# Optimization experiments

Measured on AMD Instinct MI355X. Metric: run time of the kernel, lower is better.

## Reference

```python
import jax, jax.numpy as jnp
import numpy as np

DIM = 512
NUM_HEADS = 8
HEAD_DIM = DIM // NUM_HEADS


def setup_inputs() -> dict:
    key = jax.random.key(0)
    ks = jax.random.split(key, 5)
    s = 0.02
    x = jax.random.normal(ks[0], (2, 4096, DIM), dtype=jnp.float32)
    W_qkv = jax.random.normal(ks[1], (DIM, 3 * DIM), dtype=jnp.float32) * s
    b_qkv = jnp.zeros((3 * DIM,), dtype=jnp.float32)
    W_proj = jax.random.normal(ks[2], (DIM, DIM), dtype=jnp.float32) * s
    b_proj = jnp.zeros((DIM,), dtype=jnp.float32)
    return {"x": x, "W_qkv": W_qkv, "b_qkv": b_qkv, "W_proj": W_proj, "b_proj": b_proj}


def reference(x, W_qkv, b_qkv, W_proj, b_proj):
    B, N, C = x.shape
    # qkv: [B,N,3C] -> [3,B,H,N,Dh]
    qkv = (x @ W_qkv + b_qkv).reshape(B, N, 3, NUM_HEADS, HEAD_DIM)
    qkv = jnp.transpose(qkv, (2, 0, 3, 1, 4))
    q, k, v = qkv[0], qkv[1], qkv[2]
    scale = HEAD_DIM ** -0.5
    # naive full attention matrix [B,H,N,N] (faithful to source)
    attn = jnp.einsum('bhqd,bhkd->bhqk', q, k) * scale
    attn = jax.nn.softmax(attn, axis=-1)
    out = jnp.einsum('bhqk,bhkd->bhqd', attn, v)  # [B,H,N,Dh]
    out = jnp.transpose(out, (0, 2, 1, 3)).reshape(B, N, C)
    return out @ W_proj + b_proj
```

## Files before the change

### kernel.cpp

```cpp
#include <hip/hip_runtime.h>
#include <stdint.h>

typedef _Float16 f16;
typedef _Float16 f16x4 __attribute__((ext_vector_type(4)));
typedef _Float16 f16x8 __attribute__((ext_vector_type(8)));
typedef float f32x4 __attribute__((ext_vector_type(4)));
typedef float f32x16 __attribute__((ext_vector_type(16)));
typedef uint32_t u32;
typedef u32 u32x2 __attribute__((ext_vector_type(2)));
typedef u32 u32x4 __attribute__((ext_vector_type(4)));

#define NHEADS 8
#define DH 64
#define BATCH 2
#define SEQ 4096
#define CDIM 512
#define MTOT (BATCH * SEQ)
#define QSCALE 0.18033688011112042f

__device__ __forceinline__ void gload_lds16(const void* g, void* l) {
  __builtin_amdgcn_global_load_lds(
      (const __attribute__((address_space(1))) uint32_t*)g,
      (__attribute__((address_space(3))) uint32_t*)l, 16, 0, 0);
}

__device__ __forceinline__ u32 pk2(float a, float b) {
  auto h = __builtin_amdgcn_cvt_pkrtz(a, b);
  return __builtin_bit_cast(u32, h);
}

__device__ __forceinline__ void pl32swap(u32& a, u32& b) {
  asm volatile("v_permlane32_swap_b32 %0, %1" : "+v"(a), "+v"(b));
}

__global__ void cvt_f32_f16(const float* __restrict__ in, f16* __restrict__ outp, int n) {
  int i = (blockIdx.x * 256 + threadIdx.x) * 4;
  if (i < n) {
    float4 v = *(const float4*)(in + i);
    f16x4 o = {(f16)v.x, (f16)v.y, (f16)v.z, (f16)v.w};
    *(f16x4*)(outp + i) = o;
  }
}

__global__ void cvt_transpose(const float* __restrict__ src, f16* __restrict__ dst, int Kd, int Nd) {
  int i = blockIdx.x * 256 + threadIdx.x;
  if (i < Kd * Nd) {
    int k = i / Nd, n = i - k * Nd;
    dst[(size_t)n * Kd + k] = (f16)src[i];
  }
}

template <int MODE>
__global__ __launch_bounds__(256) void gemm_f16(
    const f16* __restrict__ A, const f16* __restrict__ Bt,
    const float* __restrict__ bias, int Ncols,
    f16* __restrict__ Qo, f16* __restrict__ Ko, f16* __restrict__ Vo,
    float* __restrict__ Fo) {
  const int K = CDIM;
  const int nTN = Ncols >> 7;
  const int bm = blockIdx.x / nTN, bn = blockIdx.x % nTN;
  const int M0 = bm << 7, N0 = bn << 7;
  __shared__ __align__(16) char ldsA[128 * 64 * 2];
  __shared__ __align__(16) char ldsB[128 * 64 * 2];
  const int t = threadIdx.x;
  const int w = t >> 6, lane = t & 63;
  const int wr = w >> 1, wc = w & 1;
  const int lm = lane & 15, lk = lane >> 4;
  f32x4 acc[4][4] = {};

  const int srow = t >> 3;
  const int sj = t & 7;

  for (int k0 = 0; k0 < K; k0 += 64) {
    __syncthreads();
#pragma unroll
    for (int q = 0; q < 4; ++q) {
      int row = (q << 5) + srow;
      int col = (sj ^ (row & 7)) << 3;
      gload_lds16(A + (size_t)(M0 + row) * K + k0 + col,
                  ldsA + ((q << 8) + (w << 6)) * 16);
      gload_lds16(Bt + (size_t)(N0 + row) * K + k0 + col,
                  ldsB + ((q << 8) + (w << 6)) * 16);
    }
    asm volatile("s_waitcnt vmcnt(0)" ::: "memory");
    __syncthreads();
#pragma unroll
    for (int h = 0; h < 2; ++h) {
      f16x8 af[4], bf[4];
#pragma unroll
      for (int mi = 0; mi < 4; ++mi) {
        int row = (wr << 6) + (mi << 4) + lm;
        int slot = ((h << 2) + lk) ^ (row & 7);
        af[mi] = *(const f16x8*)(ldsA + row * 128 + slot * 16);
      }
#pragma unroll
      for (int ni = 0; ni < 4; ++ni) {
        int row = (wc << 6) + (ni << 4) + lm;
        int slot = ((h << 2) + lk) ^ (row & 7);
        bf[ni] = *(const f16x8*)(ldsB + row * 128 + slot * 16);
      }
#pragma unroll
      for (int mi = 0; mi < 4; ++mi)
#pragma unroll
        for (int ni = 0; ni < 4; ++ni)
          acc[mi][ni] = __builtin_amdgcn_mfma_f32_16x16x32_f16(af[mi], bf[ni], acc[mi][ni], 0, 0, 0);
    }
  }

  const int cbase = N0 + (wc << 6);
  if (MODE == 0) {
    const int tsec = cbase >> 9;
    const int hh = (cbase & 511) >> 6;
#pragma unroll
    for (int mi = 0; mi < 4; ++mi)
#pragma unroll
      for (int ni = 0; ni < 4; ++ni) {
        int c = cbase + (ni << 4) + lm;
        int d = c & 63;
        float bv = bias[c];
#pragma unroll
        for (int r = 0; r < 4; ++r) {
          int m = M0 + (wr << 6) + (mi << 4) + (lk << 2) + r;
          float v = acc[mi][ni][r] + bv;
          int bb = m >> 12, tok = m & 4095;
          size_t bh = (size_t)bb * NHEADS + hh;
          if (tsec == 0)      Qo[(bh * SEQ + tok) * DH + d] = (f16)(v * QSCALE);
          else if (tsec == 1) Ko[(bh * SEQ + tok) * DH + d] = (f16)v;
          else                Vo[(bh * DH + d) * SEQ + tok] = (f16)v;
        }
      }
  } else {
#pragma unroll
    for (int mi = 0; mi < 4; ++mi)
#pragma unroll
      for (int ni = 0; ni < 4; ++ni) {
        int c = cbase + (ni << 4) + lm;
        float bv = bias[c];
#pragma unroll
        for (int r = 0; r < 4; ++r) {
          int m = M0 + (wr << 6) + (mi << 4) + (lk << 2) + r;
          Fo[(size_t)m * CDIM + c] = acc[mi][ni][r] + bv;
        }
      }
  }
}

__global__ __launch_bounds__(256, 2) void attn_f16(
    const f16* __restrict__ Qw, const f16* __restrict__ Kw,
    const f16* __restrict__ Vw, f16* __restrict__ Ao) {
  const int bh = blockIdx.x >> 5;
  const int qt = blockIdx.x & 31;
  const int t = threadIdx.x, lane = t & 63;
  const int l31 = lane & 31, hi = lane >> 5;
  const int w = t >> 6;
  const int p = w & 1;
  const int wq = w >> 1;
  __shared__ __align__(16) char lds[65536];
  const int qbase = (qt << 7) + (wq << 6);
  const int qA = qbase + l31;
  const int qB = qbase + 32 + l31;
  const f16* QbA = Qw + ((size_t)bh * SEQ + qA) * DH;
  const f16* QbB = Qw + ((size_t)bh * SEQ + qB) * DH;
  f16x8 qfA[4], qfB[4];
#pragma unroll
  for (int cd = 0; cd < 4; ++cd) {
    qfA[cd] = *(const f16x8*)(QbA + cd * 16 + hi * 8);
    qfB[cd] = *(const f16x8*)(QbB + cd * 16 + hi * 8);
  }
  f32x16 oA0 = {}, oA1 = {}, oB0 = {}, oB1 = {};
  float lA = 0.f, lB = 0.f;
  const f16* Kb = Kw + (size_t)bh * SEQ * DH;
  const f16* Vb = Vw + (size_t)bh * DH * SEQ;
  const int srow = t >> 3, sj = t & 7;

#define STAGE(buf, kv0_)                                                      \
  {                                                                           \
    _Pragma("unroll") for (int q2 = 0; q2 < 2; ++q2) {                        \
      const int row = (q2 << 5) + srow;                                       \
      const int col = (sj ^ (row & 7)) << 3;                                  \
      gload_lds16(Kb + (size_t)((kv0_) + row) * DH + col,                     \
                  lds + (buf) * 16384 + row * 128 + sj * 16);                 \
      gload_lds16(Vb + (size_t)row * SEQ + (kv0_) + col,                      \
                  lds + 32768 + (buf) * 16384 + row * 128 + sj * 16);         \
    }                                                                         \
  }

  STAGE(0, 0);
  __syncthreads();

#pragma unroll 2
  for (int tt = 0; tt < 64; ++tt) {
    const int cur = tt & 1;
    const char* Kc = lds + cur * 16384;
    const char* Vc = lds + 32768 + cur * 16384;
    if (tt < 63) STAGE(cur ^ 1, (tt + 1) << 6);

    f16x8 kf[4];
    const int krow = (p << 5) + l31;
#pragma unroll
    for (int cd = 0; cd < 4; ++cd)
      kf[cd] = *(const f16x8*)(Kc + krow * 128 + ((((cd << 1) | hi) ^ (l31 & 7)) << 4));

    f32x16 sA = {}, sB = {};
#pragma unroll
    for (int cd = 0; cd < 4; ++cd) {
      sA = __builtin_amdgcn_mfma_f32_32x32x16_f16(kf[cd], qfA[cd], sA, 0, 0, 0);
      sB = __builtin_amdgcn_mfma_f32_32x32x16_f16(kf[cd], qfB[cd], sB, 0, 0, 0);
    }

    f16x8 pfA[2], pfB[2];
#define SOFTMAX(s, l, pf)                                                     \
    {                                                                         \
      _Pragma("unroll") for (int i = 0; i < 16; ++i)                          \
          s[i] = __builtin_amdgcn_exp2f(s[i]);                                \
      float a8[8];                                                            \
      _Pragma("unroll") for (int i = 0; i < 8; ++i) a8[i] = s[i] + s[i + 8];  \
      l += ((a8[0] + a8[1]) + (a8[2] + a8[3])) +                              \
           ((a8[4] + a8[5]) + (a8[6] + a8[7]));                               \
      _Pragma("unroll") for (int c = 0; c < 2; ++c) {                         \
        u32 a0 = pk2(s[8 * c + 0], s[8 * c + 1]);                             \
        u32 a1 = pk2(s[8 * c + 2], s[8 * c + 3]);                             \
        u32 b0 = pk2(s[8 * c + 4], s[8 * c + 5]);                             \
        u32 b1 = pk2(s[8 * c + 6], s[8 * c + 7]);                             \
        pl32swap(a0, b0);                                                     \
        pl32swap(a1, b1);                                                     \
        u32x4 pw = {a0, a1, b0, b1};                                          \
        pf[c] = __builtin_bit_cast(f16x8, pw);                                \
      }                                                                       \
    }
    SOFTMAX(sA, lA, pfA);
    SOFTMAX(sB, lB, pfB);

    f16x8 vf0[2], vf1[2];
#pragma unroll
    for (int c2 = 0; c2 < 2; ++c2) {
      const int ck = (p << 1) | c2;
      const int sl = (((ck << 1) | hi) ^ (l31 & 7)) << 4;
      vf0[c2] = *(const f16x8*)(Vc + l31 * 128 + sl);
      vf1[c2] = *(const f16x8*)(Vc + (32 + l31) * 128 + sl);
    }
#pragma unroll
    for (int c2 = 0; c2 < 2; ++c2) {
      oA0 = __builtin_amdgcn_mfma_f32_32x32x16_f16(vf0[c2], pfA[c2], oA0, 0, 0, 0);
      oA1 = __builtin_amdgcn_mfma_f32_32x32x16_f16(vf1[c2], pfA[c2], oA1, 0, 0, 0);
      oB0 = __builtin_amdgcn_mfma_f32_32x32x16_f16(vf0[c2], pfB[c2], oB0, 0, 0, 0);
      oB1 = __builtin_amdgcn_mfma_f32_32x32x16_f16(vf1[c2], pfB[c2], oB1, 0, 0, 0);
    }
    __syncthreads();
  }

  float* ob = (float*)(lds) + (((wq << 6) + lane) << 5);
  float* mlb = (float*)(lds + 16384) + ((wq << 6) + lane);
  const int b_ = bh >> 3, h_ = bh & 7;

#define MERGE_WRITE(o0, o1, l, myq)                                           \
    {                                                                         \
      if (p) {                                                                \
        *(f32x16*)ob = o0;                                                    \
        *(f32x16*)(ob + 16) = o1;                                             \
        mlb[0] = l;                                                           \
      }                                                                       \
      __syncthreads();                                                        \
      if (!p) {                                                               \
        f32x16 po0 = *(const f32x16*)ob;                                      \
        f32x16 po1 = *(const f32x16*)(ob + 16);                               \
        float lt = l + mlb[0];                                                \
        lt += __shfl_xor(lt, 32);                                             \
        float inv = 1.0f / lt;                                                \
        f16* orow = Ao + ((size_t)b_ * SEQ + (myq)) * CDIM + (h_ << 6) + (hi << 2); \
        _Pragma("unroll") for (int u = 0; u < 4; ++u) {                       \
          float e0 = (o0[4 * u] + po0[4 * u]) * inv;                          \
          float e1 = (o0[4 * u + 1] + po0[4 * u + 1]) * inv;                  \
          float e2 = (o0[4 * u + 2] + po0[4 * u + 2]) * inv;                  \
          float e3 = (o0[4 * u + 3] + po0[4 * u + 3]) * inv;                  \
          u32x2 pa = {pk2(e0, e1), pk2(e2, e3)};                              \
          *reinterpret_cast<u32x2*>(orow + (u << 3)) = pa;                    \
          float f0 = (o1[4 * u] + po1[4 * u]) * inv;                          \
          float f1 = (o1[4 * u + 1] + po1[4 * u + 1]) * inv;                  \
          float f2 = (o1[4 * u + 2] + po1[4 * u + 2]) * inv;                  \
          float f3 = (o1[4 * u + 3] + po1[4 * u + 3]) * inv;                  \
          u32x2 pb = {pk2(f0, f1), pk2(f2, f3)};                              \
          *reinterpret_cast<u32x2*>(orow + 32 + (u << 3)) = pb;               \
        }                                                                     \
      }                                                                       \
      __syncthreads();                                                        \
    }

  MERGE_WRITE(oA0, oA1, lA, qA);
  MERGE_WRITE(oB0, oB1, lB, qB);
}

extern "C" void kernel_launch(void* const* d_in, const int* in_sizes, int n_in,
                              void* d_out, int out_size, void* d_ws, size_t ws_size,
                              hipStream_t stream) {
  const float* x = (const float*)d_in[0];
  const float* Wqkv = (const float*)d_in[1];
  const float* bqkv = (const float*)d_in[2];
  const float* Wproj = (const float*)d_in[3];
  const float* bproj = (const float*)d_in[4];
  float* out = (float*)d_out;
  char* ws = (char*)d_ws;

  const size_t SZ_X = (size_t)MTOT * CDIM * 2;
  f16* xb = (f16*)(ws);
  f16* attno = xb;
  f16* wqkvT = (f16*)(ws + SZ_X);
  f16* wprojT = (f16*)(ws + SZ_X + (size_t)1536 * 512 * 2);
  f16* Qwv = (f16*)(ws + SZ_X + (size_t)1536 * 512 * 2 + (size_t)512 * 512 * 2);
  f16* Kwv = (f16*)((char*)Qwv + SZ_X);
  f16* Vwv = (f16*)((char*)Kwv + SZ_X);

  cvt_f32_f16<<<(MTOT * CDIM / 4 + 255) / 256, 256, 0, stream>>>(x, xb, MTOT * CDIM);
  cvt_transpose<<<(512 * 1536 + 255) / 256, 256, 0, stream>>>(Wqkv, wqkvT, 512, 1536);
  cvt_transpose<<<(512 * 512 + 255) / 256, 256, 0, stream>>>(Wproj, wprojT, 512, 512);
  gemm_f16<0><<<64 * 12, 256, 0, stream>>>(xb, wqkvT, bqkv, 1536, Qwv, Kwv, Vwv, nullptr);
  attn_f16<<<16 * 32, 256, 0, stream>>>(Qwv, Kwv, Vwv, attno);
  gemm_f16<1><<<64 * 4, 256, 0, stream>>>(attno, wprojT, bproj, 512, nullptr, nullptr, nullptr, out);
}
```

Before: 151.1 us.

## Fuse prep kernels with tiled transpose, remap blocks per XCD, vectorize V stores

Replaces the three conversion launches with one prep kernel that converts x and transposes both weight matrices through a padded LDS tile, so reads and writes are coalesced. Remaps block indices in both GEMMs and the attention kernel so that blocks sharing data run on the same XCD, aiming at better L2 reuse. Vectorizes the transposed V store in the QKV GEMM epilogue to 4-wide f16 writes. This removes two launches and the strided scalar transpose writes, but the prep kernel is longer and the remapping assumes the grid size divides by 8.

```diff
diff --git a/kernel.cpp b/kernel.cpp
--- a/kernel.cpp
+++ b/kernel.cpp
@@ -33,20 +33,45 @@
   asm volatile("v_permlane32_swap_b32 %0, %1" : "+v"(a), "+v"(b));
 }
 
-__global__ void cvt_f32_f16(const float* __restrict__ in, f16* __restrict__ outp, int n) {
-  int i = (blockIdx.x * 256 + threadIdx.x) * 4;
-  if (i < n) {
-    float4 v = *(const float4*)(in + i);
+__device__ __forceinline__ void tr64(const float* __restrict__ src,
+                                     f16* __restrict__ dst, int k0, int n0,
+                                     int Ns, int Ks, f16* L) {
+  const int t = threadIdx.x;
+#pragma unroll
+  for (int i = 0; i < 8; ++i) {
+    int idx = (i * 256 + t) * 2;
+    int r = idx >> 6, c = idx & 63;
+    float2 v = *(const float2*)(src + (size_t)(k0 + r) * Ns + n0 + c);
+    L[c * 66 + r] = (f16)v.x;
+    L[(c + 1) * 66 + r] = (f16)v.y;
+  }
+  __syncthreads();
+#pragma unroll
+  for (int i = 0; i < 8; ++i) {
+    int idx = (i * 256 + t) * 2;
+    int r = idx >> 6, c = idx & 63;
+    *(u32*)(dst + (size_t)(n0 + r) * Ks + k0 + c) = *(const u32*)(L + r * 66 + c);
+  }
+}
+
+__global__ void prep(const float* __restrict__ x, f16* __restrict__ xb,
+                     const float* __restrict__ Wqkv, f16* __restrict__ wqkvT,
+                     const float* __restrict__ Wproj, f16* __restrict__ wprojT) {
+  __shared__ f16 L[64 * 66];
+  const int b = blockIdx.x;
+  if (b < 4096) {
+    int i = (b * 256 + (int)threadIdx.x) * 4;
+    float4 v = *(const float4*)(x + i);
     f16x4 o = {(f16)v.x, (f16)v.y, (f16)v.z, (f16)v.w};
-    *(f16x4*)(outp + i) = o;
-  }
-}
-
-__global__ void cvt_transpose(const float* __restrict__ src, f16* __restrict__ dst, int Kd, int Nd) {
-  int i = blockIdx.x * 256 + threadIdx.x;
-  if (i < Kd * Nd) {
-    int k = i / Nd, n = i - k * Nd;
-    dst[(size_t)n * Kd + k] = (f16)src[i];
+    *(f16x4*)(xb + i) = o;
+  } else if (b < 4096 + 192) {
+    int tw = b - 4096;
+    int kt = tw / 24, nt = tw % 24;
+    tr64(Wqkv, wqkvT, kt << 6, nt << 6, 1536, 512, L);
+  } else {
+    int tw = b - 4096 - 192;
+    int kt = tw >> 3, nt = tw & 7;
+    tr64(Wproj, wprojT, kt << 6, nt << 6, 512, 512, L);
   }
 }
 
@@ -58,7 +83,9 @@
     float* __restrict__ Fo) {
   const int K = CDIM;
   const int nTN = Ncols >> 7;
-  const int bm = blockIdx.x / nTN, bn = blockIdx.x % nTN;
+  const int cpx = gridDim.x >> 3;
+  const int vb = (blockIdx.x & 7) * cpx + (blockIdx.x >> 3);
+  const int bm = vb / nTN, bn = vb % nTN;
   const int M0 = bm << 7, N0 = bn << 7;
   __shared__ __align__(16) char ldsA[128 * 64 * 2];
   __shared__ __align__(16) char ldsB[128 * 64 * 2];
@@ -118,15 +145,22 @@
         int c = cbase + (ni << 4) + lm;
         int d = c & 63;
         float bv = bias[c];
-#pragma unroll
-        for (int r = 0; r < 4; ++r) {
-          int m = M0 + (wr << 6) + (mi << 4) + (lk << 2) + r;
-          float v = acc[mi][ni][r] + bv;
-          int bb = m >> 12, tok = m & 4095;
-          size_t bh = (size_t)bb * NHEADS + hh;
-          if (tsec == 0)      Qo[(bh * SEQ + tok) * DH + d] = (f16)(v * QSCALE);
-          else if (tsec == 1) Ko[(bh * SEQ + tok) * DH + d] = (f16)v;
-          else                Vo[(bh * DH + d) * SEQ + tok] = (f16)v;
+        if (tsec == 2) {
+          int m0 = M0 + (wr << 6) + (mi << 4) + (lk << 2);
+          int bb = m0 >> 12, tok = m0 & 4095;
+          f16x4 vv = {(f16)(acc[mi][ni][0] + bv), (f16)(acc[mi][ni][1] + bv),
+                      (f16)(acc[mi][ni][2] + bv), (f16)(acc[mi][ni][3] + bv)};
+          *(f16x4*)(Vo + ((size_t)(bb * NHEADS + hh) * DH + d) * SEQ + tok) = vv;
+        } else {
+#pragma unroll
+          for (int r = 0; r < 4; ++r) {
+            int m = M0 + (wr << 6) + (mi << 4) + (lk << 2) + r;
+            float v = acc[mi][ni][r] + bv;
+            int bb = m >> 12, tok = m & 4095;
+            size_t bh = (size_t)bb * NHEADS + hh;
+            if (tsec == 0) Qo[(bh * SEQ + tok) * DH + d] = (f16)(v * QSCALE);
+            else           Ko[(bh * SEQ + tok) * DH + d] = (f16)v;
+          }
         }
       }
   } else {
@@ -148,8 +182,9 @@
 __global__ __launch_bounds__(256, 2) void attn_f16(
     const f16* __restrict__ Qw, const f16* __restrict__ Kw,
     const f16* __restrict__ Vw, f16* __restrict__ Ao) {
-  const int bh = blockIdx.x >> 5;
-  const int qt = blockIdx.x & 31;
+  const int vb = ((blockIdx.x & 7) << 6) + (blockIdx.x >> 3);
+  const int bh = vb >> 5;
+  const int qt = vb & 31;
   const int t = threadIdx.x, lane = t & 63;
   const int l31 = lane & 31, hi = lane >> 5;
   const int w = t >> 6;
@@ -310,9 +345,7 @@
   f16* Kwv = (f16*)((char*)Qwv + SZ_X);
   f16* Vwv = (f16*)((char*)Kwv + SZ_X);
 
-  cvt_f32_f16<<<(MTOT * CDIM / 4 + 255) / 256, 256, 0, stream>>>(x, xb, MTOT * CDIM);
-  cvt_transpose<<<(512 * 1536 + 255) / 256, 256, 0, stream>>>(Wqkv, wqkvT, 512, 1536);
-  cvt_transpose<<<(512 * 512 + 255) / 256, 256, 0, stream>>>(Wproj, wprojT, 512, 512);
+  prep<<<4096 + 192 + 64, 256, 0, stream>>>(x, xb, Wqkv, wqkvT, Wproj, wprojT);
   gemm_f16<0><<<64 * 12, 256, 0, stream>>>(xb, wqkvT, bqkv, 1536, Qwv, Kwv, Vwv, nullptr);
   attn_f16<<<16 * 32, 256, 0, stream>>>(Qwv, Kwv, Vwv, attno);
   gemm_f16<1><<<64 * 4, 256, 0, stream>>>(attno, wprojT, bproj, 512, nullptr, nullptr, nullptr, out);
```

Result: faster. 128.8 us (-14.8%).
